# Performance work log

Hardware: AMD Instinct MI355X
Metric: run time of the kernel (lower is better)

The kernel has to match this reference:

```python
import jax, jax.numpy as jnp
import numpy as np

EPS = 1e-7  # keras_backend.epsilon()
ROUTINGS = 3


def setup_inputs() -> dict:
    key = jax.random.key(0)
    k1, k2, k3, k4, k5 = jax.random.split(key, 5)
    B, H, W, I, O = 32, 8, 8, 32, 64
    return {
        "inputs_poses": jax.random.normal(k1, (B, H, W, I, 4, 4), dtype=jnp.float32),
        "inputs_activations": jax.random.uniform(k2, (B, H, W, I), dtype=jnp.float32),
        "w": jax.random.normal(k3, (I, O, 4, 4), dtype=jnp.float32),
        "beta_v": jax.random.normal(k4, (1, O), dtype=jnp.float32),
        "beta_a": jax.random.normal(k5, (1, O), dtype=jnp.float32),
    }


def _em_routing(votes, i_act, beta_v, beta_a, routings):
    # votes: [B, N, O, 16], i_act: [B, N]
    B, N, O, P = votes.shape
    act = i_act[..., None, None]              # [B, N, 1, 1]
    bv = beta_v[..., None, :, None]           # [1, 1, O, 1]
    ba = beta_a[..., None, :, None]           # [1, 1, O, 1]
    rr = jnp.full((N, O, 1), 1.0 / O, dtype=votes.dtype)
    it_min, it_max = 1.0, min(routings, 3.0)
    o_mean = o_act = None
    for it in range(routings):
        inv_temp = it_min + (it_max - it_min) * it / max(1.0, routings - 1.0)
        # ---- m-step ----
        rr_prime = rr * act                                    # [B, N, O, 1]
        rps = rr_prime.sum(axis=-3, keepdims=True)             # [B, 1, O, 1]
        o_mean = (rr_prime * votes).sum(axis=-3, keepdims=True) / rps   # [B,1,O,16]
        o_stdv = jnp.sqrt((rr_prime * jnp.square(votes - o_mean)).sum(axis=-3, keepdims=True) / rps)
        o_cost_h = (bv + jnp.log(o_stdv + EPS)) * rps          # [B,1,O,16]
        o_cost = o_cost_h.sum(axis=-1, keepdims=True)          # [B,1,O,1]
        o_cost_mean = o_cost.mean(axis=-2, keepdims=True)      # [B,1,1,1]
        o_cost_stdv = jnp.sqrt(jnp.square(o_cost - o_cost_mean).sum(axis=-2, keepdims=True) / O)
        o_act = jax.nn.sigmoid(inv_temp * (ba + (o_cost_mean - o_cost) / (o_cost_stdv + EPS)))
        # ---- e-step ----
        if it < routings - 1:
            o_p = (-jnp.sum(jnp.square(votes - o_mean) / (2.0 * jnp.square(o_stdv)), axis=-1, keepdims=True)
                   - jnp.sum(jnp.log(o_stdv + EPS), axis=-1, keepdims=True))   # [B,N,O,1]
            zz = jnp.log(o_act + EPS) + o_p
            rr = jax.nn.softmax(zz, axis=-2)                   # softmax over O
    poses = jnp.squeeze(o_mean, axis=-3)                       # [B, O, 16]
    activations = jnp.squeeze(o_act, axis=(-3, -1))            # [B, O]
    return poses, activations


def reference(inputs_poses, inputs_activations, w, beta_v, beta_a):
    B, H, W, I = inputs_activations.shape
    O = w.shape[1]
    # mat_transform: per-(input-type, class) 4x4 pose transform -> votes
    pose = inputs_poses.reshape(B * H * W, I, 4, 4)
    votes = jnp.einsum('siab,iobc->sioac', pose, w)            # [BHW, I, O, 4, 4]
    votes = votes.reshape(B, H, W, I, O, 16)
    # coord_addition: add scaled spatial coords to components 0 (h) and 1 (w)
    ch = jnp.zeros((1, H, 1, 1, 1, 16), votes.dtype).at[..., 0].set(
        ((jnp.arange(H, dtype=votes.dtype) + 0.5) / H).reshape(1, H, 1, 1, 1))
    cw = jnp.zeros((1, 1, W, 1, 1, 16), votes.dtype).at[..., 1].set(
        ((jnp.arange(W, dtype=votes.dtype) + 0.5) / W).reshape(1, 1, W, 1, 1))
    votes = votes + ch + cw
    votes = votes.reshape(B, H * W * I, O, 16)
    i_act = inputs_activations.reshape(B, H * W * I)
    poses, activations = _em_routing(votes, i_act, beta_v, beta_a, ROUTINGS)
    poses = poses.reshape(B, O, 4, 4)
    return poses, activations
```

## Files before the change

### kernel.cpp

```cpp
#include <hip/hip_runtime.h>


#define NB 32
#define NN 2048
#define NO 64
#define NP 16
#define EPSF 1e-7f

#define SITES_PB 8
#define IS_PB 4
#define PAIRS_PB (SITES_PB * IS_PB)

#define ACC_SLOTS 33
#define ACC_PER_B (ACC_SLOTS * NO)
#define ACC_TOTAL (NB * ACC_PER_B)

template <bool FIRST>
__global__ __launch_bounds__(256) void accum_kernel(
    const float* __restrict__ pose,
    const float* __restrict__ act,
    const float* __restrict__ wmat,
    const float* __restrict__ beta_v,
    const float* __restrict__ beta_a,
    const float* __restrict__ accum_prev,
    float* __restrict__ accum_out,
    float inv_temp)
{
    __shared__ float pose_s[PAIRS_PB * 16];
    __shared__ float act_s[PAIRS_PB];
    __shared__ float red[2][ACC_PER_B];

    const int b = blockIdx.y;
    const int sg = blockIdx.x >> 3;
    const int ig = blockIdx.x & 7;
    const int s0 = sg * SITES_PB;
    const int i0 = ig * IS_PB;
    const int tid = threadIdx.x;
    const int wv = tid >> 6;
    const int o = tid & 63;

    {
        if (tid < PAIRS_PB * 4) {
            const int pair = tid >> 2, qw = tid & 3;
            const int sl = pair >> 2, li = pair & 3;
            const size_t n = (size_t)b * NN + (s0 + sl) * 32 + (i0 + li);
            ((float4*)pose_s)[pair * 4 + qw] =
                ((const float4*)(pose + n * 16))[qw];
        }
        if (tid < PAIRS_PB) {
            const int sl = tid >> 2, li = tid & 3;
            act_s[tid] = act[(size_t)b * NN + (s0 + sl) * 32 + (i0 + li)];
        }
    }

    const float4* wp = (const float4*)(wmat + (((size_t)(i0 + wv)) * 64 + o) * 16);
    float4 w0 = wp[0], w1 = wp[1], w2 = wp[2], w3 = wp[3];

    float m[16], i2v[16], zzb = 0.f;
    if (!FIRST) {
        const float* ap = accum_prev + (size_t)b * ACC_PER_B;
        float rps = ap[32 * 64 + o];
        float rinv = 1.0f / rps;
        float logsum = 0.f;
        #pragma unroll
        for (int p = 0; p < 16; p++) {
            float mm = ap[p * 64 + o] * rinv;
            float vv = fmaxf(ap[(16 + p) * 64 + o] * rinv - mm * mm, 0.f);
            m[p] = mm;
            i2v[p] = 0.5f / vv;
            logsum += __logf(sqrtf(vv) + EPSF);
        }
        float cost = rps * (16.0f * beta_v[o] + logsum);
        float cm = cost;
        #pragma unroll
        for (int s = 32; s > 0; s >>= 1) cm += __shfl_xor(cm, s, 64);
        cm *= (1.0f / 64.0f);
        float dd = cost - cm;
        float cs = dd * dd;
        #pragma unroll
        for (int s = 32; s > 0; s >>= 1) cs += __shfl_xor(cs, s, 64);
        cs = sqrtf(cs * (1.0f / 64.0f));
        float x = inv_temp * (beta_a[o] + (cm - cost) / (cs + EPSF));
        float oa = 1.0f / (1.0f + __expf(-x));
        zzb = __logf(oa + EPSF) - logsum;
    }
    __syncthreads();

    float accR = 0.f, acc1[16], acc2[16];
    #pragma unroll
    for (int p = 0; p < 16; p++) { acc1[p] = 0.f; acc2[p] = 0.f; }

    for (int sl = 0; sl < 8; sl++) {
        const int site = s0 + sl;
        const float c0 = ((site >> 3) + 0.5f) * 0.125f;
        const float c1 = ((site & 7) + 0.5f) * 0.125f;
        const float* pr = pose_s + (sl * 4 + wv) * 16;

        float v[16];
        #pragma unroll
        for (int a = 0; a < 4; a++) {
            float pa0 = pr[a * 4 + 0], pa1 = pr[a * 4 + 1];
            float pa2 = pr[a * 4 + 2], pa3 = pr[a * 4 + 3];
            v[a * 4 + 0] = pa0 * w0.x + pa1 * w1.x + pa2 * w2.x + pa3 * w3.x;
            v[a * 4 + 1] = pa0 * w0.y + pa1 * w1.y + pa2 * w2.y + pa3 * w3.y;
            v[a * 4 + 2] = pa0 * w0.z + pa1 * w1.z + pa2 * w2.z + pa3 * w3.z;
            v[a * 4 + 3] = pa0 * w0.w + pa1 * w1.w + pa2 * w2.w + pa3 * w3.w;
        }
        v[0] += c0;
        v[1] += c1;

        float rr;
        if (FIRST) {
            rr = 1.0f / 64.0f;
        } else {
            float d = zzb;
            #pragma unroll
            for (int p = 0; p < 16; p++) {
                float t = v[p] - m[p];
                d -= t * t * i2v[p];
            }
            float mx = d;
            #pragma unroll
            for (int s = 32; s > 0; s >>= 1) mx = fmaxf(mx, __shfl_xor(mx, s, 64));
            float e = __expf(d - mx);
            float sum = e;
            #pragma unroll
            for (int s = 32; s > 0; s >>= 1) sum += __shfl_xor(sum, s, 64);
            rr = e / sum;
        }
        float rp = rr * act_s[sl * 4 + wv];
        accR += rp;
        #pragma unroll
        for (int p = 0; p < 16; p++) {
            acc1[p] += rp * v[p];
            acc2[p] += rp * v[p] * v[p];
        }
    }

    if (wv >= 2) {
        float* r = red[wv - 2];
        r[32 * 64 + o] = accR;
        #pragma unroll
        for (int p = 0; p < 16; p++) r[p * 64 + o] = acc1[p];
        #pragma unroll
        for (int p = 0; p < 16; p++) r[(16 + p) * 64 + o] = acc2[p];
    }
    __syncthreads();
    if (wv < 2) {
        const float* r = red[wv];
        accR += r[32 * 64 + o];
        #pragma unroll
        for (int p = 0; p < 16; p++) acc1[p] += r[p * 64 + o];
        #pragma unroll
        for (int p = 0; p < 16; p++) acc2[p] += r[(16 + p) * 64 + o];
    }
    __syncthreads();
    if (wv == 1) {
        float* r = red[0];
        r[32 * 64 + o] = accR;
        #pragma unroll
        for (int p = 0; p < 16; p++) r[p * 64 + o] = acc1[p];
        #pragma unroll
        for (int p = 0; p < 16; p++) r[(16 + p) * 64 + o] = acc2[p];
    }
    __syncthreads();
    if (wv == 0) {
        const float* r = red[0];
        accR += r[32 * 64 + o];
        #pragma unroll
        for (int p = 0; p < 16; p++) acc1[p] += r[p * 64 + o];
        #pragma unroll
        for (int p = 0; p < 16; p++) acc2[p] += r[(16 + p) * 64 + o];

        float* ac = accum_out + (size_t)b * ACC_PER_B;
        atomicAdd(ac + 32 * 64 + o, accR);
        #pragma unroll
        for (int p = 0; p < 16; p++) atomicAdd(ac + p * 64 + o, acc1[p]);
        #pragma unroll
        for (int p = 0; p < 16; p++) atomicAdd(ac + (16 + p) * 64 + o, acc2[p]);
    }
}

__global__ __launch_bounds__(64) void stats_final(
    const float* __restrict__ accum,
    const float* __restrict__ beta_v,
    const float* __restrict__ beta_a,
    float* __restrict__ out,
    float inv_temp)
{
    const int b = blockIdx.x;
    const int o = threadIdx.x;
    const float* ac = accum + (size_t)b * ACC_PER_B;

    float rps = ac[32 * 64 + o];
    float rinv = 1.0f / rps;
    float m[16];
    float logsum = 0.f;
    #pragma unroll
    for (int p = 0; p < 16; p++) {
        float mm = ac[p * 64 + o] * rinv;
        float vv = fmaxf(ac[(16 + p) * 64 + o] * rinv - mm * mm, 0.f);
        m[p] = mm;
        logsum += __logf(sqrtf(vv) + EPSF);
    }
    float cost = rps * (16.0f * beta_v[o] + logsum);

    float cm = cost;
    #pragma unroll
    for (int s = 32; s > 0; s >>= 1) cm += __shfl_xor(cm, s, 64);
    cm *= (1.0f / 64.0f);
    float dd = cost - cm;
    float cs = dd * dd;
    #pragma unroll
    for (int s = 32; s > 0; s >>= 1) cs += __shfl_xor(cs, s, 64);
    cs = sqrtf(cs * (1.0f / 64.0f));

    float x = inv_temp * (beta_a[o] + (cm - cost) / (cs + EPSF));
    float oa = 1.0f / (1.0f + __expf(-x));

    float* op = out + ((size_t)b * 64 + o) * 16;
    #pragma unroll
    for (int p = 0; p < 16; p++) op[p] = m[p];
    out[(size_t)NB * NO * NP + (size_t)b * 64 + o] = oa;
}

extern "C" void kernel_launch(void* const* d_in, const int* in_sizes, int n_in,
                              void* d_out, int out_size, void* d_ws, size_t ws_size,
                              hipStream_t stream) {
    const float* pose   = (const float*)d_in[0];
    const float* act    = (const float*)d_in[1];
    const float* wmat   = (const float*)d_in[2];
    const float* beta_v = (const float*)d_in[3];
    const float* beta_a = (const float*)d_in[4];
    float* out = (float*)d_out;
    float* ws = (float*)d_ws;

    float* a0 = ws;
    float* a1 = ws + (size_t)ACC_TOTAL;
    float* a2 = ws + 2 * (size_t)ACC_TOTAL;

    hipMemsetAsync(ws, 0, 3 * (size_t)ACC_TOTAL * sizeof(float), stream);

    dim3 grid(64, NB);
    accum_kernel<true ><<<grid, 256, 0, stream>>>(pose, act, wmat, beta_v, beta_a,
                                                  nullptr, a0, 0.0f);
    accum_kernel<false><<<grid, 256, 0, stream>>>(pose, act, wmat, beta_v, beta_a,
                                                  a0, a1, 1.0f);
    accum_kernel<false><<<grid, 256, 0, stream>>>(pose, act, wmat, beta_v, beta_a,
                                                  a1, a2, 2.0f);
    stats_final<<<NB, 64, 0, stream>>>(a2, beta_v, beta_a, out, 3.0f);
}
```

Before: 165.1 us.

## Use 1024-thread blocks, compute routing stats once per block, drop shared-memory reduction

Each block now covers 16 input capsule types with 16 waves instead of 4 types with 4 waves, so the grid shrinks from 64x32 to 16x32 blocks. The per-output statistics from the previous iteration are computed by one wave and shared through LDS rather than recomputed by every wave. The tree reduction of partial sums in shared memory is removed, and every wave issues its own atomics directly to global memory. The aim is to cut redundant stats work and reduction syncs, at the cost of four times more global atomics per block, more register pressure under launch_bounds(1024), and fewer blocks in flight.

```diff
diff --git a/kernel.cpp b/kernel.cpp
--- a/kernel.cpp
+++ b/kernel.cpp
@@ -8,7 +8,7 @@
 #define EPSF 1e-7f
 
 #define SITES_PB 8
-#define IS_PB 4
+#define IS_PB 16
 #define PAIRS_PB (SITES_PB * IS_PB)
 
 #define ACC_SLOTS 33
@@ -16,7 +16,7 @@
 #define ACC_TOTAL (NB * ACC_PER_B)
 
 template <bool FIRST>
-__global__ __launch_bounds__(256) void accum_kernel(
+__global__ __launch_bounds__(1024) void accum_kernel(
     const float* __restrict__ pose,
     const float* __restrict__ act,
     const float* __restrict__ wmat,
@@ -28,47 +28,44 @@
 {
     __shared__ float pose_s[PAIRS_PB * 16];
     __shared__ float act_s[PAIRS_PB];
-    __shared__ float red[2][ACC_PER_B];
+    __shared__ float stats_s[ACC_PER_B];
 
     const int b = blockIdx.y;
-    const int sg = blockIdx.x >> 3;
-    const int ig = blockIdx.x & 7;
+    const int sg = blockIdx.x >> 1;
+    const int ig = blockIdx.x & 1;
     const int s0 = sg * SITES_PB;
-    const int i0 = ig * IS_PB;
     const int tid = threadIdx.x;
-    const int wv = tid >> 6;
+    const int w = tid >> 6;
     const int o = tid & 63;
-
-    {
-        if (tid < PAIRS_PB * 4) {
-            const int pair = tid >> 2, qw = tid & 3;
-            const int sl = pair >> 2, li = pair & 3;
-            const size_t n = (size_t)b * NN + (s0 + sl) * 32 + (i0 + li);
-            ((float4*)pose_s)[pair * 4 + qw] =
-                ((const float4*)(pose + n * 16))[qw];
-        }
-        if (tid < PAIRS_PB) {
-            const int sl = tid >> 2, li = tid & 3;
-            act_s[tid] = act[(size_t)b * NN + (s0 + sl) * 32 + (i0 + li)];
-        }
-    }
-
-    const float4* wp = (const float4*)(wmat + (((size_t)(i0 + wv)) * 64 + o) * 16);
+    const int i = ig * 16 + w;
+
+    const float4* wp = (const float4*)(wmat + ((size_t)i * 64 + o) * 16);
     float4 w0 = wp[0], w1 = wp[1], w2 = wp[2], w3 = wp[3];
 
-    float m[16], i2v[16], zzb = 0.f;
-    if (!FIRST) {
+    if (tid < PAIRS_PB * 4) {
+        const int pr = tid >> 2, qw = tid & 3;
+        const int sl = pr >> 4, li = pr & 15;
+        const size_t n = (size_t)b * NN + (s0 + sl) * 32 + ig * 16 + li;
+        ((float4*)pose_s)[pr * 4 + qw] = ((const float4*)(pose + n * 16))[qw];
+    } else if (tid < PAIRS_PB * 4 + PAIRS_PB) {
+        const int t = tid - PAIRS_PB * 4;
+        const int sl = t >> 4, li = t & 15;
+        act_s[t] = act[(size_t)b * NN + (s0 + sl) * 32 + ig * 16 + li];
+    }
+
+    if (!FIRST && tid < 64) {
         const float* ap = accum_prev + (size_t)b * ACC_PER_B;
         float rps = ap[32 * 64 + o];
         float rinv = 1.0f / rps;
         float logsum = 0.f;
+        float mm[16], vv[16];
         #pragma unroll
         for (int p = 0; p < 16; p++) {
-            float mm = ap[p * 64 + o] * rinv;
-            float vv = fmaxf(ap[(16 + p) * 64 + o] * rinv - mm * mm, 0.f);
-            m[p] = mm;
-            i2v[p] = 0.5f / vv;
-            logsum += __logf(sqrtf(vv) + EPSF);
+            float mv = ap[p * 64 + o] * rinv;
+            float va = fmaxf(ap[(16 + p) * 64 + o] * rinv - mv * mv, 0.f);
+            mm[p] = mv;
+            vv[p] = va;
+            logsum += __logf(sqrtf(va) + EPSF);
         }
         float cost = rps * (16.0f * beta_v[o] + logsum);
         float cm = cost;
@@ -82,9 +79,22 @@
         cs = sqrtf(cs * (1.0f / 64.0f));
         float x = inv_temp * (beta_a[o] + (cm - cost) / (cs + EPSF));
         float oa = 1.0f / (1.0f + __expf(-x));
-        zzb = __logf(oa + EPSF) - logsum;
+        #pragma unroll
+        for (int p = 0; p < 16; p++) stats_s[p * 64 + o] = mm[p];
+        #pragma unroll
+        for (int p = 0; p < 16; p++) stats_s[(16 + p) * 64 + o] = 0.5f / vv[p];
+        stats_s[32 * 64 + o] = __logf(oa + EPSF) - logsum;
     }
     __syncthreads();
+
+    float m[16], i2v[16], zzb = 0.f;
+    if (!FIRST) {
+        #pragma unroll
+        for (int p = 0; p < 16; p++) m[p] = stats_s[p * 64 + o];
+        #pragma unroll
+        for (int p = 0; p < 16; p++) i2v[p] = stats_s[(16 + p) * 64 + o];
+        zzb = stats_s[32 * 64 + o];
+    }
 
     float accR = 0.f, acc1[16], acc2[16];
     #pragma unroll
@@ -94,7 +104,7 @@
         const int site = s0 + sl;
         const float c0 = ((site >> 3) + 0.5f) * 0.125f;
         const float c1 = ((site & 7) + 0.5f) * 0.125f;
-        const float* pr = pose_s + (sl * 4 + wv) * 16;
+        const float* pr = pose_s + (sl * 16 + w) * 16;
 
         float v[16];
         #pragma unroll
@@ -128,7 +138,7 @@
             for (int s = 32; s > 0; s >>= 1) sum += __shfl_xor(sum, s, 64);
             rr = e / sum;
         }
-        float rp = rr * act_s[sl * 4 + wv];
+        float rp = rr * act_s[sl * 16 + w];
         accR += rp;
         #pragma unroll
         for (int p = 0; p < 16; p++) {
@@ -137,48 +147,12 @@
         }
     }
 
-    if (wv >= 2) {
-        float* r = red[wv - 2];
-        r[32 * 64 + o] = accR;
-        #pragma unroll
-        for (int p = 0; p < 16; p++) r[p * 64 + o] = acc1[p];
-        #pragma unroll
-        for (int p = 0; p < 16; p++) r[(16 + p) * 64 + o] = acc2[p];
-    }
-    __syncthreads();
-    if (wv < 2) {
-        const float* r = red[wv];
-        accR += r[32 * 64 + o];
-        #pragma unroll
-        for (int p = 0; p < 16; p++) acc1[p] += r[p * 64 + o];
-        #pragma unroll
-        for (int p = 0; p < 16; p++) acc2[p] += r[(16 + p) * 64 + o];
-    }
-    __syncthreads();
-    if (wv == 1) {
-        float* r = red[0];
-        r[32 * 64 + o] = accR;
-        #pragma unroll
-        for (int p = 0; p < 16; p++) r[p * 64 + o] = acc1[p];
-        #pragma unroll
-        for (int p = 0; p < 16; p++) r[(16 + p) * 64 + o] = acc2[p];
-    }
-    __syncthreads();
-    if (wv == 0) {
-        const float* r = red[0];
-        accR += r[32 * 64 + o];
-        #pragma unroll
-        for (int p = 0; p < 16; p++) acc1[p] += r[p * 64 + o];
-        #pragma unroll
-        for (int p = 0; p < 16; p++) acc2[p] += r[(16 + p) * 64 + o];
-
-        float* ac = accum_out + (size_t)b * ACC_PER_B;
-        atomicAdd(ac + 32 * 64 + o, accR);
-        #pragma unroll
-        for (int p = 0; p < 16; p++) atomicAdd(ac + p * 64 + o, acc1[p]);
-        #pragma unroll
-        for (int p = 0; p < 16; p++) atomicAdd(ac + (16 + p) * 64 + o, acc2[p]);
-    }
+    float* ac = accum_out + (size_t)b * ACC_PER_B;
+    atomicAdd(ac + 32 * 64 + o, accR);
+    #pragma unroll
+    for (int p = 0; p < 16; p++) atomicAdd(ac + p * 64 + o, acc1[p]);
+    #pragma unroll
+    for (int p = 0; p < 16; p++) atomicAdd(ac + (16 + p) * 64 + o, acc2[p]);
 }
 
 __global__ __launch_bounds__(64) void stats_final(
@@ -241,12 +215,12 @@
 
     hipMemsetAsync(ws, 0, 3 * (size_t)ACC_TOTAL * sizeof(float), stream);
 
-    dim3 grid(64, NB);
-    accum_kernel<true ><<<grid, 256, 0, stream>>>(pose, act, wmat, beta_v, beta_a,
-                                                  nullptr, a0, 0.0f);
-    accum_kernel<false><<<grid, 256, 0, stream>>>(pose, act, wmat, beta_v, beta_a,
-                                                  a0, a1, 1.0f);
-    accum_kernel<false><<<grid, 256, 0, stream>>>(pose, act, wmat, beta_v, beta_a,
-                                                  a1, a2, 2.0f);
+    dim3 grid(16, NB);
+    accum_kernel<true ><<<grid, 1024, 0, stream>>>(pose, act, wmat, beta_v, beta_a,
+                                                   nullptr, a0, 0.0f);
+    accum_kernel<false><<<grid, 1024, 0, stream>>>(pose, act, wmat, beta_v, beta_a,
+                                                   a0, a1, 1.0f);
+    accum_kernel<false><<<grid, 1024, 0, stream>>>(pose, act, wmat, beta_v, beta_a,
+                                                   a1, a2, 2.0f);
     stats_final<<<NB, 64, 0, stream>>>(a2, beta_v, beta_a, out, 3.0f);
 }
```

Measured after the change: 273.6 us. 65.8% more time.
